# Optimization experiments

Hardware: AMD Instinct MI355X
Metric: run time of the kernel (lower is better)

## Reference

```python
import jax, jax.numpy as jnp
import numpy as np

B, S, D, H = 4, 4096, 1024, 16
DH = D // H


def setup_inputs() -> dict:
    key = jax.random.key(0)
    ks = jax.random.split(key, 8)
    scale = 1.0 / np.sqrt(D)
    return {
        "q": jax.random.normal(ks[0], (B, S, D), jnp.float32),
        "k": jax.random.normal(ks[1], (B, S, D), jnp.float32),
        "v": jax.random.normal(ks[2], (B, S, D), jnp.float32),
        "mask": jax.random.uniform(ks[3], (H, H), jnp.float32),
        # torch nn.Linear weights, layout [out, in]; applied as x @ W.T
        "Wq": jax.random.normal(ks[4], (D, D), jnp.float32) * scale,
        "Wk": jax.random.normal(ks[5], (D, D), jnp.float32) * scale,
        "Wv": jax.random.normal(ks[6], (D, D), jnp.float32) * scale,
        "Wo": jax.random.normal(ks[7], (D, D), jnp.float32) * scale,
    }


def reference(q, k, v, mask, Wq, Wk, Wv, Wo):
    # projections (bias-free Linear): x @ W.T, then split to [B,S,H,DH]
    qh = (q @ Wq.T).reshape(B, S, H, DH)
    kh = (k @ Wk.T).reshape(B, S, H, DH)
    vh = (v @ Wv.T).reshape(B, S, H, DH)
    # Faithful to source: NO head/seq transpose, so attention is over the
    # head axis per token: score [B,S,H,H]
    score = jnp.einsum('bshd,bsgd->bshg', qh, kh) / np.sqrt(DH)
    score = score * mask  # multiplicative mask, broadcast [H,H]
    p = jax.nn.softmax(score, axis=-1)
    attn = jnp.einsum('bshg,bsgd->bshd', p, vh)  # [B,S,H,DH]
    out = attn.reshape(B, S, D) @ Wo.T
    return out
```

## Files before the change

### kernel.cpp

```cpp
#include <hip/hip_runtime.h>
#include <hip/hip_bf16.h>
#include <stdint.h>


namespace {
constexpr int kD  = 1024;
constexpr int kH  = 16;
constexpr int kDH = 64;
constexpr int kM  = 4 * 4096;
constexpr size_t PER = (size_t)kM * kD;
constexpr size_t WSZ = (size_t)kD * kD;

typedef __attribute__((ext_vector_type(4))) float f32x4;
typedef __attribute__((ext_vector_type(8))) short s16x8;

__device__ __forceinline__ unsigned short f2b(float f) {
  uint32_t x = __builtin_bit_cast(uint32_t, f);
  x += 0x7fffu + ((x >> 16) & 1u);
  return (unsigned short)(x >> 16);
}
__device__ __forceinline__ float b2f(unsigned short u) {
  return __builtin_bit_cast(float, (uint32_t)u << 16);
}

typedef __attribute__((address_space(3))) void as3_void;
typedef __attribute__((address_space(1))) void as1_void;
__device__ __forceinline__ void gload_lds16(const void* g, void* l) {
  __builtin_amdgcn_global_load_lds((const as1_void*)(uintptr_t)g,
                                   (as3_void*)(uint32_t)(uintptr_t)l, 16, 0, 0);
}

__global__ __launch_bounds__(256) void cvt_bf16(
    const float* __restrict__ q, const float* __restrict__ k, const float* __restrict__ v,
    const float* __restrict__ Wq, const float* __restrict__ Wk, const float* __restrict__ Wv,
    const float* __restrict__ Wo, unsigned short* __restrict__ out) {
  const size_t total8 = (3 * PER + 4 * WSZ) / 8;
  for (size_t i8 = (size_t)blockIdx.x * blockDim.x + threadIdx.x; i8 < total8;
       i8 += (size_t)gridDim.x * blockDim.x) {
    size_t i = i8 * 8;
    const float* s; size_t o;
    if (i < 3 * PER) {
      if (i < PER)            { s = q; o = i; }
      else if (i < 2 * PER)   { s = k; o = i - PER; }
      else                    { s = v; o = i - 2 * PER; }
    } else {
      size_t j = i - 3 * PER;
      if (j < WSZ)            { s = Wq; o = j; }
      else if (j < 2 * WSZ)   { s = Wk; o = j - WSZ; }
      else if (j < 3 * WSZ)   { s = Wv; o = j - 2 * WSZ; }
      else                    { s = Wo; o = j - 3 * WSZ; }
    }
    f32x4 f0 = ((const f32x4*)(s + o))[0];
    f32x4 f1 = ((const f32x4*)(s + o))[1];
    s16x8 r;
#pragma unroll
    for (int d = 0; d < 4; ++d) {
      r[d]     = (short)f2b(f0[d]);
      r[4 + d] = (short)f2b(f1[d]);
    }
    *(s16x8*)(out + i) = r;
  }
}

constexpr int BM2 = 256, BN2 = 256, BK2 = 64;
constexpr int KT2 = kD / BK2;

__device__ __forceinline__ void mfma16(f32x4 (&a)[2][4], s16x8 (&af)[2][2],
                                       s16x8 (&bw)[4][2]) {
  __builtin_amdgcn_s_setprio(1);
#pragma unroll
  for (int mi = 0; mi < 2; ++mi)
#pragma unroll
    for (int nj = 0; nj < 4; ++nj)
#pragma unroll
      for (int kk = 0; kk < 2; ++kk)
        a[mi][nj] = __builtin_amdgcn_mfma_f32_16x16x32_bf16(af[mi][kk], bw[nj][kk],
                                                            a[mi][nj], 0, 0, 0);
  __builtin_amdgcn_s_setprio(0);
}

template <bool OUT_F32>
__device__ __forceinline__ void gemmq_body(const unsigned short* __restrict__ A,
                                           const unsigned short* __restrict__ Bm,
                                           void* __restrict__ Cp) {
  constexpr int K = kD, N = kD;
  __shared__ __align__(16) unsigned short lds[65536];

  const int lin = blockIdx.y * gridDim.x + blockIdx.x;
  const int xcd = lin & 7;
  const int idx = lin >> 3;
  const int m0 = (xcd * 8 + (idx >> 2)) * BM2;
  const int n0 = (idx & 3) * BN2;

  const int t    = threadIdx.x;
  const int lane = t & 63;
  const int w    = t >> 6;
  const int wrow = w >> 1;
  const int wcol = w & 1;

  const int srow  = lane >> 3;
  const int sslot = (lane & 7) ^ srow;
  const int fr     = lane & 15;
  const int fkslot = lane >> 4;

  auto stageHalf = [&](const unsigned short* src, int grow0, int k0, int slot) {
    const unsigned short* g = src + (size_t)(grow0 + w * 16 + srow) * K + k0 + sslot * 8;
    unsigned short* l = lds + slot * 8192 + w * 16 * 64;
    gload_lds16(g, l);
    gload_lds16(g + (size_t)8 * K, l + 8 * 64);
  };
  auto rdA = [&](int slot, int mi, int kk) -> s16x8 {
    int r = wrow * 32 + mi * 16 + fr;
    int s16 = (kk * 4 + fkslot) ^ (r & 7);
    return *(const s16x8*)(lds + slot * 8192 + r * 64 + s16 * 8);
  };
  auto rdB = [&](int slot, int nj, int kk) -> s16x8 {
    int r = wcol * 64 + nj * 16 + fr;
    int s16 = (kk * 4 + fkslot) ^ (r & 7);
    return *(const s16x8*)(lds + slot * 8192 + r * 64 + s16 * 8);
  };

  f32x4 acc[4][2][4];
#pragma unroll
  for (int qi = 0; qi < 4; ++qi)
#pragma unroll
    for (int mi = 0; mi < 2; ++mi)
#pragma unroll
      for (int nj = 0; nj < 4; ++nj) acc[qi][mi][nj] = (f32x4){0.f, 0.f, 0.f, 0.f};

  stageHalf(A,  m0,       0, 0);
  stageHalf(Bm, n0,       0, 2);
  stageHalf(Bm, n0 + 128, 0, 3);
  stageHalf(A,  m0 + 128, 0, 1);
  stageHalf(A,  m0,       BK2, 4);
  stageHalf(Bm, n0 + 128, BK2, 7);

  s16x8 af[2][2], bw[4][2];

  for (int tt = 0; tt < KT2; ++tt) {
    const int b  = (tt & 1) * 4;
    const int nb = b ^ 4;
    const int k1 = (tt + 1) * BK2;
    const int k2 = (tt + 2) * BK2;

    if (tt == 0)            { asm volatile("s_waitcnt vmcnt(8)" ::: "memory"); }
    else if (tt == KT2 - 1) { asm volatile("s_waitcnt vmcnt(0)" ::: "memory"); }
    else                    { asm volatile("s_waitcnt vmcnt(4)" ::: "memory"); }
    __builtin_amdgcn_s_barrier();
#pragma unroll
    for (int mi = 0; mi < 2; ++mi)
#pragma unroll
      for (int kk = 0; kk < 2; ++kk) af[mi][kk] = rdA(b + 0, mi, kk);
#pragma unroll
    for (int nj = 0; nj < 4; ++nj)
#pragma unroll
      for (int kk = 0; kk < 2; ++kk) bw[nj][kk] = rdB(b + 2, nj, kk);
    if (tt + 1 < KT2) {
      stageHalf(A,  m0 + 128, k1, nb + 1);
      stageHalf(Bm, n0,       k1, nb + 2);
    }
    asm volatile("s_waitcnt lgkmcnt(0)" ::: "memory");
    __builtin_amdgcn_sched_barrier(0);
    mfma16(acc[0], af, bw);

    if (tt == 0) { asm volatile("s_waitcnt vmcnt(8)" ::: "memory"); }
    else         { asm volatile("s_waitcnt vmcnt(4)" ::: "memory"); }
    __builtin_amdgcn_s_barrier();
#pragma unroll
    for (int nj = 0; nj < 4; ++nj)
#pragma unroll
      for (int kk = 0; kk < 2; ++kk) bw[nj][kk] = rdB(b + 3, nj, kk);
    asm volatile("s_waitcnt lgkmcnt(0)" ::: "memory");
    __builtin_amdgcn_sched_barrier(0);
    mfma16(acc[1], af, bw);

    __builtin_amdgcn_s_barrier();
#pragma unroll
    for (int mi = 0; mi < 2; ++mi)
#pragma unroll
      for (int kk = 0; kk < 2; ++kk) af[mi][kk] = rdA(b + 1, mi, kk);
    if (tt + 2 < KT2) stageHalf(A, m0, k2, b + 0);
    asm volatile("s_waitcnt lgkmcnt(0)" ::: "memory");
    __builtin_amdgcn_sched_barrier(0);
    mfma16(acc[2], af, bw);

    __builtin_amdgcn_s_barrier();
#pragma unroll
    for (int nj = 0; nj < 4; ++nj)
#pragma unroll
      for (int kk = 0; kk < 2; ++kk) bw[nj][kk] = rdB(b + 2, nj, kk);
    if (tt + 2 < KT2) stageHalf(Bm, n0 + 128, k2, b + 3);
    asm volatile("s_waitcnt lgkmcnt(0)" ::: "memory");
    __builtin_amdgcn_sched_barrier(0);
    mfma16(acc[3], af, bw);
  }

  constexpr int MH[4] = {0, 0, 1, 1};
  constexpr int NH[4] = {0, 1, 1, 0};
  const int cr = (lane >> 4) * 4;
  const int cc = lane & 15;
#pragma unroll
  for (int qi = 0; qi < 4; ++qi)
#pragma unroll
    for (int mi = 0; mi < 2; ++mi)
#pragma unroll
      for (int nj = 0; nj < 4; ++nj)
#pragma unroll
        for (int r = 0; r < 4; ++r) {
          size_t row = (size_t)(m0 + MH[qi] * 128 + wrow * 32 + mi * 16 + cr + r);
          size_t col = (size_t)(n0 + NH[qi] * 128 + wcol * 64 + nj * 16 + cc);
          if constexpr (OUT_F32)
            ((float*)Cp)[row * N + col] = acc[qi][mi][nj][r];
          else
            ((unsigned short*)Cp)[row * N + col] = f2b(acc[qi][mi][nj][r]);
        }
}

__global__ __launch_bounds__(512, 2) void proj_gemmq(
    const unsigned short* __restrict__ qb, const unsigned short* __restrict__ kb,
    const unsigned short* __restrict__ vb, const unsigned short* __restrict__ Wqb,
    const unsigned short* __restrict__ Wkb, const unsigned short* __restrict__ Wvb,
    unsigned short* __restrict__ qh, unsigned short* __restrict__ kh,
    unsigned short* __restrict__ vh) {
  const unsigned short *A, *W;
  unsigned short* C;
  if (blockIdx.z == 0)      { A = qb; W = Wqb; C = qh; }
  else if (blockIdx.z == 1) { A = kb; W = Wkb; C = kh; }
  else                      { A = vb; W = Wvb; C = vh; }
  gemmq_body<false>(A, W, C);
}

__global__ __launch_bounds__(512, 2) void out_gemmq(const unsigned short* __restrict__ attn,
                                                    const unsigned short* __restrict__ Wob,
                                                    float* __restrict__ out) {
  gemmq_body<true>(attn, Wob, out);
}

__global__ __launch_bounds__(256) void attn_tok(const unsigned short* __restrict__ qh,
                                                const unsigned short* __restrict__ kh,
                                                const unsigned short* __restrict__ vh,
                                                const float* __restrict__ mask,
                                                unsigned short* __restrict__ attn) {
  __shared__ float P[4][16][17];
  __shared__ __align__(16) unsigned short Vs[4][16 * 64];
  const int lane = threadIdx.x & 63;
  const int wid  = threadIdx.x >> 6;
  const size_t tok = (size_t)blockIdx.x * 4 + wid;

  const unsigned short* qp = qh + tok * kD;
  const unsigned short* kp = kh + tok * kD;
  const unsigned short* vp = vh + tok * kD;

  {
    const s16x8* src = (const s16x8*)vp;
    s16x8 a = src[2 * lane], b = src[2 * lane + 1];
    s16x8* dst = (s16x8*)Vs[wid];
    dst[2 * lane] = a;
    dst[2 * lane + 1] = b;
  }

  const int fr = lane & 15;
  const int fk = (lane >> 4) * 8;
  s16x8 a0 = *(const s16x8*)(qp + fr * kDH + fk);
  s16x8 a1 = *(const s16x8*)(qp + fr * kDH + 32 + fk);
  s16x8 b0 = *(const s16x8*)(kp + fr * kDH + fk);
  s16x8 b1 = *(const s16x8*)(kp + fr * kDH + 32 + fk);
  f32x4 s = {0.f, 0.f, 0.f, 0.f};
  s = __builtin_amdgcn_mfma_f32_16x16x32_bf16(a0, b0, s, 0, 0, 0);
  s = __builtin_amdgcn_mfma_f32_16x16x32_bf16(a1, b1, s, 0, 0, 0);

  const int cr = (lane >> 4) * 4;
  const int cc = lane & 15;
  float p[4];
#pragma unroll
  for (int r = 0; r < 4; ++r) {
    float val = s[r] * 0.125f * mask[(cr + r) * kH + cc];
    float mx = val;
#pragma unroll
    for (int d = 1; d < 16; d <<= 1) mx = fmaxf(mx, __shfl_xor(mx, d));
    float e = __expf(val - mx);
    float sum = e;
#pragma unroll
    for (int d = 1; d < 16; d <<= 1) sum += __shfl_xor(sum, d);
    p[r] = e / sum;
  }
#pragma unroll
  for (int r = 0; r < 4; ++r) P[wid][cr + r][cc] = p[r];

  const int h  = lane >> 2;
  const int d0 = (lane & 3) * 16;
  float o[16];
#pragma unroll
  for (int i = 0; i < 16; ++i) o[i] = 0.f;
#pragma unroll
  for (int g = 0; g < 16; ++g) {
    float pg = P[wid][h][g];
    s16x8 v0 = *(const s16x8*)(Vs[wid] + g * kDH + d0);
    s16x8 v1 = *(const s16x8*)(Vs[wid] + g * kDH + d0 + 8);
#pragma unroll
    for (int dd = 0; dd < 8; ++dd) {
      o[dd]     += pg * b2f((unsigned short)v0[dd]);
      o[8 + dd] += pg * b2f((unsigned short)v1[dd]);
    }
  }
  unsigned short* op = attn + tok * kD + h * kDH + d0;
  s16x8 r0, r1;
#pragma unroll
  for (int dd = 0; dd < 8; ++dd) {
    r0[dd] = (short)f2b(o[dd]);
    r1[dd] = (short)f2b(o[dd + 8]);
  }
  *(s16x8*)op = r0;
  *(s16x8*)(op + 8) = r1;
}

constexpr int BM = 128, BN = 128, BK = 32;
constexpr int LDSP = BK + 8;
__device__ __forceinline__ void cvt16_store(const float* __restrict__ g, short* __restrict__ l) {
  const f32x4* s4 = (const f32x4*)g;
  f32x4 f0 = s4[0], f1 = s4[1], f2 = s4[2], f3 = s4[3];
  s16x8 o0, o1;
#pragma unroll
  for (int i = 0; i < 4; ++i) {
    o0[i]     = (short)f2b(f0[i]);
    o0[4 + i] = (short)f2b(f1[i]);
    o1[i]     = (short)f2b(f2[i]);
    o1[4 + i] = (short)f2b(f3[i]);
  }
  *(s16x8*)l = o0;
  *(s16x8*)(l + 8) = o1;
}

template <bool A_BF16, bool OUT_F32>
__device__ __forceinline__ void gemm_body_cvt(const void* __restrict__ Ap,
                                              const float* __restrict__ Wp,
                                              void* __restrict__ Cp) {
  constexpr int N = kD, K = kD;
  __shared__ short As[BM * LDSP];
  __shared__ short Bs[BN * LDSP];
  const int t  = threadIdx.x;
  const int m0 = blockIdx.y * BM;
  const int n0 = blockIdx.x * BN;
  const int srow = t >> 1;
  const int scol = (t & 1) * 16;
  const int lane = t & 63;
  const int wid  = t >> 6;
  const int wm   = (wid >> 1) * 64;
  const int wn   = (wid & 1) * 64;
  const int fr   = lane & 15;
  const int fk   = (lane >> 4) * 8;

  f32x4 acc[4][4];
#pragma unroll
  for (int i = 0; i < 4; ++i)
#pragma unroll
    for (int j = 0; j < 4; ++j) acc[i][j] = (f32x4){0.f, 0.f, 0.f, 0.f};

  for (int k0 = 0; k0 < K; k0 += BK) {
    if constexpr (A_BF16) {
      const unsigned short* Ab = (const unsigned short*)Ap;
      const s16x8* src = (const s16x8*)(Ab + (size_t)(m0 + srow) * K + k0 + scol);
      s16x8 v0 = src[0], v1 = src[1];
      *(s16x8*)(As + srow * LDSP + scol) = v0;
      *(s16x8*)(As + srow * LDSP + scol + 8) = v1;
    } else {
      cvt16_store((const float*)Ap + (size_t)(m0 + srow) * K + k0 + scol,
                  As + srow * LDSP + scol);
    }
    cvt16_store(Wp + (size_t)(n0 + srow) * K + k0 + scol, Bs + srow * LDSP + scol);
    __syncthreads();
    s16x8 af[4], bw[4];
#pragma unroll
    for (int i = 0; i < 4; ++i)
      af[i] = *(const s16x8*)(As + (wm + i * 16 + fr) * LDSP + fk);
#pragma unroll
    for (int j = 0; j < 4; ++j)
      bw[j] = *(const s16x8*)(Bs + (wn + j * 16 + fr) * LDSP + fk);
#pragma unroll
    for (int i = 0; i < 4; ++i)
#pragma unroll
      for (int j = 0; j < 4; ++j)
        acc[i][j] = __builtin_amdgcn_mfma_f32_16x16x32_bf16(af[i], bw[j], acc[i][j], 0, 0, 0);
    __syncthreads();
  }
  const int cr = (lane >> 4) * 4;
  const int cc = lane & 15;
#pragma unroll
  for (int i = 0; i < 4; ++i)
#pragma unroll
    for (int j = 0; j < 4; ++j)
#pragma unroll
      for (int r = 0; r < 4; ++r) {
        size_t row = (size_t)(m0 + wm + i * 16 + cr + r);
        size_t col = (size_t)(n0 + wn + j * 16 + cc);
        if constexpr (OUT_F32)
          ((float*)Cp)[row * N + col] = acc[i][j][r];
        else
          ((unsigned short*)Cp)[row * N + col] = f2b(acc[i][j][r]);
      }
}

__global__ __launch_bounds__(256) void proj_gemm_cvt(
    const float* __restrict__ q, const float* __restrict__ k, const float* __restrict__ v,
    const float* __restrict__ Wq, const float* __restrict__ Wk, const float* __restrict__ Wv,
    unsigned short* __restrict__ qh, unsigned short* __restrict__ kh,
    unsigned short* __restrict__ vh) {
  const float* A; const float* W; unsigned short* C;
  if (blockIdx.z == 0)      { A = q; W = Wq; C = qh; }
  else if (blockIdx.z == 1) { A = k; W = Wk; C = kh; }
  else                      { A = v; W = Wv; C = vh; }
  gemm_body_cvt<false, false>(A, W, C);
}

__global__ __launch_bounds__(256) void out_gemm_cvt(const unsigned short* __restrict__ attn,
                                                    const float* __restrict__ Wo,
                                                    float* __restrict__ out) {
  gemm_body_cvt<true, true>(attn, Wo, out);
}

}

extern "C" void kernel_launch(void* const* d_in, const int* in_sizes, int n_in,
                              void* d_out, int out_size, void* d_ws, size_t ws_size,
                              hipStream_t stream) {
  (void)in_sizes; (void)n_in; (void)out_size;
  const float* q    = (const float*)d_in[0];
  const float* k    = (const float*)d_in[1];
  const float* v    = (const float*)d_in[2];
  const float* mask = (const float*)d_in[3];
  const float* Wq   = (const float*)d_in[4];
  const float* Wk   = (const float*)d_in[5];
  const float* Wv   = (const float*)d_in[6];
  const float* Wo   = (const float*)d_in[7];

  const size_t need = (6 * PER + 4 * WSZ) * sizeof(unsigned short);
  if (ws_size >= need) {
    unsigned short* qb  = (unsigned short*)d_ws;
    unsigned short* kb  = qb + PER;
    unsigned short* vb  = kb + PER;
    unsigned short* Wqb = vb + PER;
    unsigned short* Wkb = Wqb + WSZ;
    unsigned short* Wvb = Wkb + WSZ;
    unsigned short* Wob = Wvb + WSZ;
    unsigned short* qh  = Wob + WSZ;
    unsigned short* kh  = qh + PER;
    unsigned short* vh  = kh + PER;
    unsigned short* at  = qb;

    cvt_bf16<<<2048, 256, 0, stream>>>(q, k, v, Wq, Wk, Wv, Wo, qb);
    proj_gemmq<<<dim3(kD / BN2, kM / BM2, 3), 512, 0, stream>>>(qb, kb, vb, Wqb, Wkb, Wvb,
                                                                qh, kh, vh);
    attn_tok<<<dim3(kM / 4), 256, 0, stream>>>(qh, kh, vh, mask, at);
    out_gemmq<<<dim3(kD / BN2, kM / BM2), 512, 0, stream>>>(at, Wob, (float*)d_out);
  } else {
    unsigned short* qh = (unsigned short*)d_ws;
    unsigned short* kh = qh + PER;
    unsigned short* vh = kh + PER;
    unsigned short* at = (ws_size >= 4 * PER * sizeof(unsigned short)) ? (vh + PER) : qh;
    proj_gemm_cvt<<<dim3(kD / BN, kM / BM, 3), 256, 0, stream>>>(q, k, v, Wq, Wk, Wv,
                                                                 qh, kh, vh);
    attn_tok<<<dim3(kM / 4), 256, 0, stream>>>(qh, kh, vh, mask, at);
    out_gemm_cvt<<<dim3(kD / BN, kM / BM), 256, 0, stream>>>(at, Wo, (float*)d_out);
  }
}
```

Baseline: 224.3 us.

## Simplify GEMM pipeline to one-tile-ahead prefetch with full vmcnt wait

Replaces the two-stage-ahead prefetch schedule with fine-grained vmcnt waits by a simpler scheme: each iteration waits for all global loads, then issues the next K-tile's four half loads interleaved with the four MFMA quadrants. Quadrant traversal order changes (A0B0, A1B0, A1B1, A0B1) and the epilogue mapping is updated to match. Explicit lgkmcnt waits and sched_barriers are removed, leaving LDS-read scheduling to the compiler. This reduces prefetch depth, so global-load latency may be less well hidden.

```diff
diff --git a/kernel.cpp b/kernel.cpp
--- a/kernel.cpp
+++ b/kernel.cpp
@@ -130,23 +130,20 @@
 
   stageHalf(A,  m0,       0, 0);
   stageHalf(Bm, n0,       0, 2);
+  stageHalf(A,  m0 + 128, 0, 1);
   stageHalf(Bm, n0 + 128, 0, 3);
-  stageHalf(A,  m0 + 128, 0, 1);
-  stageHalf(A,  m0,       BK2, 4);
-  stageHalf(Bm, n0 + 128, BK2, 7);
 
   s16x8 af[2][2], bw[4][2];
 
   for (int tt = 0; tt < KT2; ++tt) {
-    const int b  = (tt & 1) * 4;
-    const int nb = b ^ 4;
-    const int k1 = (tt + 1) * BK2;
-    const int k2 = (tt + 2) * BK2;
-
-    if (tt == 0)            { asm volatile("s_waitcnt vmcnt(8)" ::: "memory"); }
-    else if (tt == KT2 - 1) { asm volatile("s_waitcnt vmcnt(0)" ::: "memory"); }
-    else                    { asm volatile("s_waitcnt vmcnt(4)" ::: "memory"); }
-    __builtin_amdgcn_s_barrier();
+    const int b    = (tt & 1) * 4;
+    const int nb   = b ^ 4;
+    const int k1   = (tt + 1) * BK2;
+    const bool more = (tt + 1 < KT2);
+
+    asm volatile("s_waitcnt vmcnt(0)" ::: "memory");
+    asm volatile("s_barrier" ::: "memory");
+    if (more) { stageHalf(A, m0, k1, nb + 0); stageHalf(Bm, n0, k1, nb + 2); }
 #pragma unroll
     for (int mi = 0; mi < 2; ++mi)
 #pragma unroll
@@ -155,48 +152,34 @@
     for (int nj = 0; nj < 4; ++nj)
 #pragma unroll
       for (int kk = 0; kk < 2; ++kk) bw[nj][kk] = rdB(b + 2, nj, kk);
-    if (tt + 1 < KT2) {
-      stageHalf(A,  m0 + 128, k1, nb + 1);
-      stageHalf(Bm, n0,       k1, nb + 2);
-    }
-    asm volatile("s_waitcnt lgkmcnt(0)" ::: "memory");
-    __builtin_amdgcn_sched_barrier(0);
     mfma16(acc[0], af, bw);
 
-    if (tt == 0) { asm volatile("s_waitcnt vmcnt(8)" ::: "memory"); }
-    else         { asm volatile("s_waitcnt vmcnt(4)" ::: "memory"); }
-    __builtin_amdgcn_s_barrier();
+    asm volatile("s_barrier" ::: "memory");
+    if (more) stageHalf(A, m0 + 128, k1, nb + 1);
+#pragma unroll
+    for (int mi = 0; mi < 2; ++mi)
+#pragma unroll
+      for (int kk = 0; kk < 2; ++kk) af[mi][kk] = rdA(b + 1, mi, kk);
+    mfma16(acc[1], af, bw);
+
+    asm volatile("s_barrier" ::: "memory");
+    if (more) stageHalf(Bm, n0 + 128, k1, nb + 3);
 #pragma unroll
     for (int nj = 0; nj < 4; ++nj)
 #pragma unroll
       for (int kk = 0; kk < 2; ++kk) bw[nj][kk] = rdB(b + 3, nj, kk);
-    asm volatile("s_waitcnt lgkmcnt(0)" ::: "memory");
-    __builtin_amdgcn_sched_barrier(0);
-    mfma16(acc[1], af, bw);
-
-    __builtin_amdgcn_s_barrier();
+    mfma16(acc[2], af, bw);
+
+    asm volatile("s_barrier" ::: "memory");
 #pragma unroll
     for (int mi = 0; mi < 2; ++mi)
 #pragma unroll
-      for (int kk = 0; kk < 2; ++kk) af[mi][kk] = rdA(b + 1, mi, kk);
-    if (tt + 2 < KT2) stageHalf(A, m0, k2, b + 0);
-    asm volatile("s_waitcnt lgkmcnt(0)" ::: "memory");
-    __builtin_amdgcn_sched_barrier(0);
-    mfma16(acc[2], af, bw);
-
-    __builtin_amdgcn_s_barrier();
-#pragma unroll
-    for (int nj = 0; nj < 4; ++nj)
-#pragma unroll
-      for (int kk = 0; kk < 2; ++kk) bw[nj][kk] = rdB(b + 2, nj, kk);
-    if (tt + 2 < KT2) stageHalf(Bm, n0 + 128, k2, b + 3);
-    asm volatile("s_waitcnt lgkmcnt(0)" ::: "memory");
-    __builtin_amdgcn_sched_barrier(0);
+      for (int kk = 0; kk < 2; ++kk) af[mi][kk] = rdA(b + 0, mi, kk);
     mfma16(acc[3], af, bw);
   }
 
-  constexpr int MH[4] = {0, 0, 1, 1};
-  constexpr int NH[4] = {0, 1, 1, 0};
+  constexpr int MH[4] = {0, 1, 1, 0};
+  constexpr int NH[4] = {0, 0, 1, 1};
   const int cr = (lane >> 4) * 4;
   const int cc = lane & 15;
 #pragma unroll
```

Result: no change. 227.8 us (+1.5%).
